# Kernel tuning notes

Measured on AMD Instinct MI355X. Metric: run time of the kernel, lower is better.

## Reference

```python
import jax, jax.numpy as jnp
import numpy as np

V, E, DZ, C = 32000, 8, 30, 10
CH = (4, 8, 8)
K = (3, 3, 3)
S = (2, 2, 1)
B, L = 512, 4096


def setup_inputs() -> dict:
    key = jax.random.key(0)
    ks = jax.random.split(key, 12)
    inp = {
        "input_ids": jax.random.randint(ks[0], (B, L), 0, V),
        "attention_mask": jnp.ones((B, L), dtype=jnp.float32),
        "z": jax.random.normal(ks[1], (DZ,), dtype=jnp.float32),
        "embed_table": jax.random.normal(ks[2], (V, E), dtype=jnp.float32),
        # ensemble-stacked frozen conv weights, torch Conv1d layout [O, I, K]
        "W1": jax.random.normal(ks[3], (DZ, CH[0], E, K[0]), dtype=jnp.float32) * 0.2,
        "b1": jax.random.normal(ks[4], (DZ, CH[0]), dtype=jnp.float32) * 0.1,
        "W2": jax.random.normal(ks[5], (DZ, CH[1], CH[0], K[1]), dtype=jnp.float32) * 0.2,
        "b2": jax.random.normal(ks[6], (DZ, CH[1]), dtype=jnp.float32) * 0.1,
        "W3": jax.random.normal(ks[7], (DZ, CH[2], CH[1], K[2]), dtype=jnp.float32) * 0.2,
        "b3": jax.random.normal(ks[8], (DZ, CH[2]), dtype=jnp.float32) * 0.1,
        "Wh": jax.random.normal(ks[9], (DZ, C, CH[2]), dtype=jnp.float32) * 0.2,
        "bh": jax.random.normal(ks[10], (DZ, C), dtype=jnp.float32) * 0.1,
    }
    return inp


def _conv1d(x, w, stride):
    # x: [B, Cin, L], w: [Cout, Cin, K]
    return jax.lax.conv_general_dilated(
        x, w, window_strides=(stride,), padding="VALID",
        dimension_numbers=("NCH", "OIH", "NCH"))


def _forward(input_ids, attention_mask, z, embed_table,
             W1, b1, W2, b2, W3, b3, Wh, bh):
    x = embed_table[input_ids]                      # [B, L, E]
    x = x * attention_mask[..., None]
    x = jnp.transpose(x, (0, 2, 1))                 # [B, E, L]

    def one_net(w1, c1, w2, c2, w3, c3, wh, ch):
        h = jax.nn.relu(_conv1d(x, w1, S[0]) + c1[None, :, None])
        h = jax.nn.relu(_conv1d(h, w2, S[1]) + c2[None, :, None])
        h = jax.nn.relu(_conv1d(h, w3, S[2]) + c3[None, :, None])
        pooled = h.mean(axis=-1)                    # [B, ch3]
        return pooled @ wh.T + ch                   # [B, C]

    pis = jax.vmap(one_net)(W1, b1, W2, b2, W3, b3, Wh, bh)  # [Dz, B, C]
    return jnp.einsum("dbc,d->bc", pis, z)          # [B, C]


def reference(input_ids, attention_mask, z, embed_table,
              W1, b1, W2, b2, W3, b3, Wh, bh):
    return _forward(input_ids, attention_mask, z, embed_table,
                    W1, b1, W2, b2, W3, b3, Wh, bh)
```

## Files before the change

### kernel.cpp

```cpp
#include <hip/hip_runtime.h>
#include <stdint.h>


typedef _Float16 f16;
typedef f16 f16x2 __attribute__((ext_vector_type(2)));
typedef f16 f16x4 __attribute__((ext_vector_type(4)));
typedef f16 f16x8 __attribute__((ext_vector_type(8)));
typedef float f32x4 __attribute__((ext_vector_type(4)));

__global__ __launch_bounds__(256) void prep_kernel(
    const int* __restrict__ ids, const float* __restrict__ mask,
    const float* __restrict__ tbl,
    const float* __restrict__ W1, const float* __restrict__ W2,
    const float* __restrict__ W3,
    f16* __restrict__ x, f16* __restrict__ a1q,
    f16* __restrict__ a2, f16* __restrict__ a3) {
  const int blk = blockIdx.x;
  if (blk < 4096) {
    const int b  = blk >> 3;
    const int l0 = ((blk & 7) * 256 + threadIdx.x) * 2;
    const int2   iv = *(const int2*)(ids + (size_t)b * 4096 + l0);
    const float2 mv = *(const float2*)(mask + (size_t)b * 4096 + l0);
    const float4* t4 = (const float4*)tbl;
    const float4 a0 = t4[(size_t)iv.x * 2], A1 = t4[(size_t)iv.x * 2 + 1];
    const float4 c0 = t4[(size_t)iv.y * 2], C1 = t4[(size_t)iv.y * 2 + 1];
    const float r0[8] = {a0.x, a0.y, a0.z, a0.w, A1.x, A1.y, A1.z, A1.w};
    const float r1[8] = {c0.x, c0.y, c0.z, c0.w, C1.x, C1.y, C1.z, C1.w};
    f16* xb = x + (size_t)b * 8 * 4096 + l0;
    #pragma unroll
    for (int e = 0; e < 8; ++e) {
      f16x2 p; p.x = (f16)(r0[e] * mv.x); p.y = (f16)(r1[e] * mv.y);
      *(f16x2*)(xb + e * 4096) = p;
    }
  } else {
    const int i = (blk - 4096) * 256 + threadIdx.x;
    if (i < 512) {
      const int g = i >> 6, l = i & 63;
      const int kg = l >> 4, col = l & 15;
      const int d = 4 * g + (col >> 2);
      f16x8 v;
      #pragma unroll
      for (int j = 0; j < 8; ++j) {
        const int e = 2 * kg + (j >> 2), tap = j & 3;
        float val = 0.0f;
        if (tap < 3 && d < 30)
          val = W1[d * 96 + (col & 3) * 24 + e * 3 + tap];
        v[j] = (f16)val;
      }
      *(f16x8*)(a1q + ((size_t)g * 64 + l) * 8) = v;
    } else if (i < 2432) {
      const int idx = i - 512, d = idx >> 6, lane = idx & 63;
      const int quad = lane >> 4, m = lane & 15;
      f16x8 v;
      #pragma unroll
      for (int j = 0; j < 8; ++j) {
        float val = 0.0f;
        if (m < 8)  { if (j < 3)           val = W2[d * 96 + m * 12 + quad * 3 + j]; }
        else        { if (j >= 2 && j < 5) val = W2[d * 96 + (m - 8) * 12 + quad * 3 + (j - 2)]; }
        v[j] = (f16)val;
      }
      *(f16x8*)(a2 + ((size_t)d * 64 + lane) * 8) = v;
    } else if (i < 4352) {
      const int idx = i - 2432, d = idx >> 6, lane = idx & 63;
      const int quad = lane >> 4, m = lane & 15;
      f16x8 v;
      #pragma unroll
      for (int j = 0; j < 8; ++j) {
        const int c2 = quad * 2 + (j >> 2), t = j & 3;
        float val = 0.0f;
        if (m < 8)  { if (t < 3)  val = W3[d * 192 + m * 24 + c2 * 3 + t]; }
        else        { if (t >= 1) val = W3[d * 192 + (m - 8) * 24 + c2 * 3 + (t - 1)]; }
        v[j] = (f16)val;
      }
      *(f16x8*)(a3 + ((size_t)d * 64 + lane) * 8) = v;
    }
  }
}

__global__ __launch_bounds__(1024, 8) void ensemble_f16_kernel(
    const f16* __restrict__ x,
    const f16* __restrict__ a1q,
    const f16* __restrict__ a2,
    const f16* __restrict__ a3,
    const float* __restrict__ z,
    const float* __restrict__ b1, const float* __restrict__ b2,
    const float* __restrict__ b3,
    const float* __restrict__ Wh, const float* __restrict__ bh,
    float* __restrict__ part)
{
  const int tid = threadIdx.x;
  const int swz = ((blockIdx.x & 7) * 512) + (blockIdx.x >> 3);
  const int b   = swz >> 3;
  const int G   = swz & 7;
  const int d_base = 4 * G;

  __shared__ __align__(16) f16 smemh[32768];
  float* red = (float*)smemh;

  const int w = tid >> 6, lane = tid & 63, quad = lane >> 4, n = lane & 15;
  const int gg = w >> 2, wv = w & 3;
  const int d  = d_base + gg;
  const int dc = d < 30 ? d : 29;

  {
    const f16x8 bw1 = *(const f16x8*)(a1q + ((size_t)G * 64 + lane) * 8);
    const int dn  = d_base + (n >> 2);
    const int dnc = dn < 30 ? dn : 29;
    const float bias = b1[dnc * 4 + (n & 3)];
    const f32x4 c1i = {bias, bias, bias, bias};
    const char* xc = (const char*)x + (size_t)b * 65536 + quad * 16384 + 4 * n;
    f16x4* h1c = (f16x4*)smemh + (n >> 2) * 2048 + (n & 3) * 512;
    const int rot1 = 5 * (n & 3);
    #pragma unroll
    for (int i = 0; i < 8; ++i) {
      const int t = w + 16 * i;
      const uint32_t o = 64u * (uint32_t)t;
      union { f16x8 v; uint32_t dw[4]; } u;
      u.dw[0] = *(const uint32_t*)(xc + o);
      u.dw[1] = *(const uint32_t*)(xc + o + 4);
      u.dw[2] = *(const uint32_t*)(xc + o + 8192);
      u.dw[3] = *(const uint32_t*)(xc + o + 8192 + 4);
      const f32x4 D = __builtin_amdgcn_mfma_f32_16x16x32_f16(u.v, bw1, c1i, 0, 0, 0);
      f16x4 p;
      p.x = (f16)fmaxf(D[0], 0.0f); p.y = (f16)fmaxf(D[1], 0.0f);
      p.z = (f16)fmaxf(D[2], 0.0f); p.w = (f16)fmaxf(D[3], 0.0f);
      const int slot = (4 * t + quad + rot1) & 511;
      h1c[slot] = p;
    }
  }
  __syncthreads();

  f32x4 Ci[8];
  {
    const f16x8 af2 = *(const f16x8*)(a2 + ((size_t)dc * 64 + lane) * 8);
    const f32x4 cinit2 = *(const f32x4*)(b2 + dc * 8 + (quad & 1) * 4);
    const f16x4* h1r = (const f16x4*)smemh + gg * 2048 + quad * 512;
    const int rot2 = 5 * quad;
    #pragma unroll
    for (int i = 0; i < 8; ++i) {
      const int t = wv + 4 * i;
      const int base = 16 * t + n;
      const f16x4 lo = h1r[(base + rot2) & 511];
      const f16x4 hi = h1r[(base + 1 + rot2) & 511];
      const f16x8 bv = __builtin_shufflevector(lo, hi, 0, 1, 2, 3, 4, 5, 6, 7);
      Ci[i] = __builtin_amdgcn_mfma_f32_16x16x32_f16(af2, bv, cinit2, 0, 0, 0);
    }
  }
  __syncthreads();

  {
    f16* h2b = smemh + gg * 8192;
    const int shift = quad >> 1;
    const int c2b   = (quad & 1) * 4;
    #pragma unroll
    for (int i = 0; i < 8; ++i) {
      const int t  = wv + 4 * i;
      const int dw = 16 * t + n;
      #pragma unroll
      for (int r = 0; r < 4; ++r) {
        const int row  = c2b + r;
        const int slot = (dw + 5 * row) & 511;
        h2b[row * 1024 + slot * 2 + shift] = (f16)fmaxf(Ci[i][r], 0.0f);
      }
    }
  }
  __syncthreads();

  float pool4[4] = {0.0f, 0.0f, 0.0f, 0.0f};
  {
    const f16x8 af3 = *(const f16x8*)(a3 + ((size_t)dc * 64 + lane) * 8);
    const f32x4 cinit3 = *(const f32x4*)(b3 + dc * 8 + (quad & 1) * 4);
    const f16* h2r = smemh + gg * 8192;
    const int c2a = quad * 2;
    const int rotA = 5 * c2a, rotB = 5 * (c2a + 1);
    #pragma unroll
    for (int i = 0; i < 8; ++i) {
      const int t  = wv + 4 * i;
      const int dw = 16 * t + n;
      union { f16x8 v; f16x2 q[4]; } u;
      u.q[0] = *(const f16x2*)(h2r + c2a * 1024       + 2 * ((dw     + rotA) & 511));
      u.q[1] = *(const f16x2*)(h2r + c2a * 1024       + 2 * ((dw + 1 + rotA) & 511));
      u.q[2] = *(const f16x2*)(h2r + (c2a + 1) * 1024 + 2 * ((dw     + rotB) & 511));
      u.q[3] = *(const f16x2*)(h2r + (c2a + 1) * 1024 + 2 * ((dw + 1 + rotB) & 511));
      const f32x4 C = __builtin_amdgcn_mfma_f32_16x16x32_f16(af3, u.v, cinit3, 0, 0, 0);
      const int pl = 32 * t + 2 * n + (quad >> 1);
      if (pl < 1021) {
        #pragma unroll
        for (int r = 0; r < 4; ++r) pool4[r] += fmaxf(C[r], 0.0f);
      }
    }
  }
  __syncthreads();

  {
    #pragma unroll
    for (int r = 0; r < 4; ++r) pool4[r] += __shfl_xor(pool4[r], 1, 64);
    #pragma unroll
    for (int r = 0; r < 4; ++r) pool4[r] += __shfl_xor(pool4[r], 2, 64);
    #pragma unroll
    for (int r = 0; r < 4; ++r) pool4[r] += __shfl_xor(pool4[r], 4, 64);
    #pragma unroll
    for (int r = 0; r < 4; ++r) pool4[r] += __shfl_xor(pool4[r], 8, 64);
    #pragma unroll
    for (int r = 0; r < 4; ++r) pool4[r] += __shfl_xor(pool4[r], 32, 64);
    if ((lane & 47) == 0) {
      const int cg = (lane >> 4) & 1;
      #pragma unroll
      for (int r = 0; r < 4; ++r)
        red[gg * 32 + wv * 8 + cg * 4 + r] = pool4[r];
    }
  }
  __syncthreads();

  if ((w & 3) == 0 && lane < 10 && d < 30) {
    float acc = bh[d * 10 + lane];
    #pragma unroll
    for (int c3 = 0; c3 < 8; ++c3) {
      const float pooled = red[gg * 32 + c3]      + red[gg * 32 + 8 + c3]
                         + red[gg * 32 + 16 + c3] + red[gg * 32 + 24 + c3];
      acc = fmaf(pooled * (1.0f / 1021.0f), Wh[d * 80 + lane * 8 + c3], acc);
    }
    part[((size_t)d * 512 + b) * 10 + lane] = z[d] * acc;
  }
}

__global__ __launch_bounds__(256) void reduce30_kernel(
    const float* __restrict__ part,
    float* __restrict__ out)
{
  const int i = blockIdx.x * 256 + threadIdx.x;
  float s = 0.0f;
  #pragma unroll
  for (int dd = 0; dd < 30; ++dd) s += part[dd * 5120 + i];
  out[i] = s;
}

__global__ __launch_bounds__(256, 6) void ensemble_kernel(
    const int* __restrict__ ids, const float* __restrict__ mask,
    const float* __restrict__ z, const float* __restrict__ tbl,
    const float* __restrict__ W1, const float* __restrict__ b1,
    const float* __restrict__ W2, const float* __restrict__ b2,
    const float* __restrict__ W3, const float* __restrict__ b3,
    const float* __restrict__ Wh, const float* __restrict__ bh,
    float* __restrict__ part)
{
  const int tid  = threadIdx.x;
  const int half = blockIdx.x & 1;
  const int bd   = blockIdx.x >> 1;
  const int b    = bd & 511;
  const int d    = bd >> 9;

  __shared__ float smem[4128];
  __shared__ float red[32];
  __shared__ float pooled[8];

  const int l_lo = half ? 1024 : 0;
  const int l_hi = half ? 2047 : 1029;
  const int j_lo = half ? 512  : 0;
  const int j_hi = half ? 1023 : 514;
  const int o_lo = half ? 512  : 0;
  const int o_hi = half ? 1021 : 512;

  const int*    idrow = ids  + (size_t)b * 4096;
  const float*  mrow  = mask + (size_t)b * 4096;
  const float4* tbl4  = (const float4*)tbl;
  const float*  w1p = W1 + d * 96;
  const float*  w2p = W2 + d * 96;
  const float*  w3p = W3 + d * 192;

  {
    float bia[4];
    #pragma unroll
    for (int c = 0; c < 4; ++c) bia[c] = b1[d * 4 + c];

    #pragma unroll 1
    for (int pass = 0; pass < 2; ++pass) {
      const int l0 = l_lo + 2 * tid + 512 * pass;
      const int p0 = 2 * l0;
      const int4   iv = *(const int4*)(idrow + p0);
      const float4 mv = *(const float4*)(mrow + p0);
      int i4; float m4;
      if (p0 + 4 < 4096) { i4 = idrow[p0 + 4]; m4 = mrow[p0 + 4]; }
      else               { i4 = 0;              m4 = 0.0f; }

      const int   pid[5] = {iv.x, iv.y, iv.z, iv.w, i4};
      const float pm[5]  = {mv.x, mv.y, mv.z, mv.w, m4};

      float a0[4], a1v[4];
      #pragma unroll
      for (int c = 0; c < 4; ++c) { a0[c] = bia[c]; a1v[c] = bia[c]; }

      #pragma unroll
      for (int q = 0; q < 5; ++q) {
        const float4 va = tbl4[(size_t)pid[q] * 2];
        const float4 vb = tbl4[(size_t)pid[q] * 2 + 1];
        const float xe[8] = {va.x * pm[q], va.y * pm[q], va.z * pm[q], va.w * pm[q],
                             vb.x * pm[q], vb.y * pm[q], vb.z * pm[q], vb.w * pm[q]};
        if (q <= 2) {
          #pragma unroll
          for (int c = 0; c < 4; ++c)
            #pragma unroll
            for (int e = 0; e < 8; ++e)
              a0[c] = fmaf(xe[e], w1p[c * 24 + e * 3 + q], a0[c]);
        }
        if (q >= 2) {
          #pragma unroll
          for (int c = 0; c < 4; ++c)
            #pragma unroll
            for (int e = 0; e < 8; ++e)
              a1v[c] = fmaf(xe[e], w1p[c * 24 + e * 3 + (q - 2)], a1v[c]);
        }
      }
      const int rel = l0 - l_lo;
      if (l0 + 1 < l_hi) {
        #pragma unroll
        for (int c = 0; c < 4; ++c)
          *(float2*)(smem + c * 1032 + rel) =
              make_float2(fmaxf(a0[c], 0.0f), fmaxf(a1v[c], 0.0f));
      } else if (l0 < l_hi) {
        #pragma unroll
        for (int c = 0; c < 4; ++c)
          smem[c * 1032 + rel] = fmaxf(a0[c], 0.0f);
      }
    }
    const int lt = l_lo + 1024 + tid;
    if (lt < l_hi) {
      float a0[4];
      #pragma unroll
      for (int c = 0; c < 4; ++c) a0[c] = bia[c];
      #pragma unroll
      for (int k = 0; k < 3; ++k) {
        const int p = 2 * lt + k;
        const int id = idrow[p];
        const float m = mrow[p];
        const float4 va = tbl4[(size_t)id * 2];
        const float4 vb = tbl4[(size_t)id * 2 + 1];
        const float xe[8] = {va.x*m, va.y*m, va.z*m, va.w*m,
                             vb.x*m, vb.y*m, vb.z*m, vb.w*m};
        #pragma unroll
        for (int cc = 0; cc < 4; ++cc)
          #pragma unroll
          for (int e = 0; e < 8; ++e)
            a0[cc] = fmaf(xe[e], w1p[cc * 24 + e * 3 + k], a0[cc]);
      }
      #pragma unroll
      for (int c = 0; c < 4; ++c)
        smem[c * 1032 + 1024 + tid] = fmaxf(a0[c], 0.0f);
    }
  }
  __syncthreads();

  float acc2[8][2], acc2t[8];
  {
    #pragma unroll
    for (int c2 = 0; c2 < 8; ++c2) {
      const float bb = b2[d * 8 + c2];
      acc2[c2][0] = bb; acc2[c2][1] = bb; acc2t[c2] = bb;
    }
    const int rel2  = 4 * tid;
    const bool tail2 = tid < (j_hi - j_lo - 512);
    #pragma unroll 1
    for (int c1 = 0; c1 < 4; ++c1) {
      float sw[8][3];
      #pragma unroll
      for (int c2 = 0; c2 < 8; ++c2)
        #pragma unroll
        for (int kk = 0; kk < 3; ++kk)
          sw[c2][kk] = w2p[c2 * 12 + c1 * 3 + kk];
      const float* hp = smem + c1 * 1032;
      const float4 h01 = *(const float4*)(hp + rel2);
      const float  h4v = hp[rel2 + 4];
      #pragma unroll
      for (int c2 = 0; c2 < 8; ++c2) {
        acc2[c2][0] = fmaf(h01.x, sw[c2][0], fmaf(h01.y, sw[c2][1],
                      fmaf(h01.z, sw[c2][2], acc2[c2][0])));
        acc2[c2][1] = fmaf(h01.z, sw[c2][0], fmaf(h01.w, sw[c2][1],
                      fmaf(h4v,   sw[c2][2], acc2[c2][1])));
      }
      if (tail2) {
        const float t0 = hp[1024 + 2 * tid], t1 = hp[1025 + 2 * tid],
                    t2 = hp[1026 + 2 * tid];
        #pragma unroll
        for (int c2 = 0; c2 < 8; ++c2)
          acc2t[c2] = fmaf(t0, sw[c2][0], fmaf(t1, sw[c2][1],
                      fmaf(t2, sw[c2][2], acc2t[c2])));
      }
    }
    #pragma unroll
    for (int c2 = 0; c2 < 8; ++c2) {
      acc2[c2][0] = fmaxf(acc2[c2][0], 0.0f);
      acc2[c2][1] = fmaxf(acc2[c2][1], 0.0f);
      acc2t[c2]   = fmaxf(acc2t[c2],   0.0f);
    }
    __syncthreads();
    const int j0 = j_lo + 2 * tid;
    const int jr = 2 * tid;
    if (j0 + 1 < j_hi) {
      #pragma unroll
      for (int c2 = 0; c2 < 8; ++c2)
        *(float2*)(smem + c2 * 516 + jr) = make_float2(acc2[c2][0], acc2[c2][1]);
    } else if (j0 < j_hi) {
      #pragma unroll
      for (int c2 = 0; c2 < 8; ++c2)
        smem[c2 * 516 + jr] = acc2[c2][0];
    }
    if (tid < (j_hi - j_lo - 512)) {
      #pragma unroll
      for (int c2 = 0; c2 < 8; ++c2)
        smem[c2 * 516 + 512 + tid] = acc2t[c2];
    }
  }
  __syncthreads();

  float acc3[8][2];
  #pragma unroll
  for (int cc = 0; cc < 8; ++cc) {
    const float bb = b3[d * 8 + cc];
    acc3[cc][0] = bb; acc3[cc][1] = bb;
  }
  {
    const int rel3 = 2 * tid;
    #pragma unroll 1
    for (int c2 = 0; c2 < 8; ++c2) {
      float sw[8][3];
      #pragma unroll
      for (int cc = 0; cc < 8; ++cc)
        #pragma unroll
        for (int kk = 0; kk < 3; ++kk)
          sw[cc][kk] = w3p[cc * 24 + c2 * 3 + kk];
      const float* hp = smem + c2 * 516;
      const float2 ha = *(const float2*)(hp + rel3);
      const float2 hb = *(const float2*)(hp + rel3 + 2);
      #pragma unroll
      for (int cc = 0; cc < 8; ++cc) {
        acc3[cc][0] = fmaf(ha.x, sw[cc][0], fmaf(ha.y, sw[cc][1],
                      fmaf(hb.x, sw[cc][2], acc3[cc][0])));
        acc3[cc][1] = fmaf(ha.y, sw[cc][0], fmaf(hb.x, sw[cc][1],
                      fmaf(hb.y, sw[cc][2], acc3[cc][1])));
      }
    }
  }
  const int i0 = o_lo + 2 * tid;
  float psum[8];
  #pragma unroll
  for (int cc = 0; cc < 8; ++cc) {
    float s = 0.0f;
    if (i0 < o_hi)     s += fmaxf(acc3[cc][0], 0.0f);
    if (i0 + 1 < o_hi) s += fmaxf(acc3[cc][1], 0.0f);
    psum[cc] = s;
  }

  const int lane = tid & 63;
  const int wid  = tid >> 6;
  #pragma unroll
  for (int c = 0; c < 8; ++c) {
    float v = psum[c];
    #pragma unroll
    for (int off = 32; off > 0; off >>= 1) v += __shfl_down(v, off, 64);
    if (lane == 0) red[wid * 8 + c] = v;
  }
  __syncthreads();
  if (tid < 8)
    pooled[tid] = red[tid] + red[8 + tid] + red[16 + tid] + red[24 + tid];
  __syncthreads();

  if (tid < 10) {
    float acc = (half == 0) ? bh[d * 10 + tid] : 0.0f;
    #pragma unroll
    for (int c3 = 0; c3 < 8; ++c3)
      acc = fmaf(pooled[c3] * (1.0f / 1021.0f), Wh[d * 80 + tid * 8 + c3], acc);
    part[(((size_t)d * 2 + half) * 512 + b) * 10 + tid] = z[d] * acc;
  }
}

__global__ __launch_bounds__(256) void reduce60_kernel(
    const float* __restrict__ part,
    float* __restrict__ out)
{
  const int i = blockIdx.x * 256 + threadIdx.x;
  float s = 0.0f;
  #pragma unroll
  for (int dd = 0; dd < 60; ++dd) s += part[dd * 5120 + i];
  out[i] = s;
}

extern "C" void kernel_launch(void* const* d_in, const int* in_sizes, int n_in,
                              void* d_out, int out_size, void* d_ws, size_t ws_size,
                              hipStream_t stream) {
  const int*   ids  = (const int*)d_in[0];
  const float* mask = (const float*)d_in[1];
  const float* z    = (const float*)d_in[2];
  const float* tbl  = (const float*)d_in[3];
  const float* W1   = (const float*)d_in[4];
  const float* b1   = (const float*)d_in[5];
  const float* W2   = (const float*)d_in[6];
  const float* b2   = (const float*)d_in[7];
  const float* W3   = (const float*)d_in[8];
  const float* b3   = (const float*)d_in[9];
  const float* Wh   = (const float*)d_in[10];
  const float* bh   = (const float*)d_in[11];
  float* out  = (float*)d_out;
  float* part = (float*)d_ws;

  const size_t part_bytes = 1228800;
  const size_t x_bytes    = (size_t)512 * 8 * 4096 * 2;
  const size_t a1_bytes   = 8192;
  const size_t a_bytes    = 30720;
  const size_t need = part_bytes + x_bytes + a1_bytes + 2 * a_bytes;

  if (ws_size >= need) {
    f16* xh  = (f16*)((char*)d_ws + part_bytes);
    f16* a1q = (f16*)((char*)d_ws + part_bytes + x_bytes);
    f16* a2  = (f16*)((char*)d_ws + part_bytes + x_bytes + a1_bytes);
    f16* a3  = (f16*)((char*)d_ws + part_bytes + x_bytes + a1_bytes + a_bytes);
    hipLaunchKernelGGL(prep_kernel, dim3(4096 + 17), dim3(256), 0, stream,
                       ids, mask, tbl, W1, W2, W3, xh, a1q, a2, a3);
    hipLaunchKernelGGL(ensemble_f16_kernel, dim3(512 * 8), dim3(1024), 0, stream,
                       xh, a1q, a2, a3, z, b1, b2, b3, Wh, bh, part);
    hipLaunchKernelGGL(reduce30_kernel, dim3(20), dim3(256), 0, stream, part, out);
  } else {
    hipLaunchKernelGGL(ensemble_kernel, dim3(512 * 30 * 2), dim3(256), 0, stream,
                       ids, mask, z, tbl, W1, b1, W2, b2, W3, b3, Wh, bh, part);
    hipLaunchKernelGGL(reduce60_kernel, dim3(20), dim3(256), 0, stream, part, out);
  }
}
```

Before: 187.2 us.

## Pre-convert embedding table to fp16 and add group term to LDS slot rotation

After: 186.3 us. No clear change (-0.5%).

```diff
diff --git a/kernel.cpp b/kernel.cpp
--- a/kernel.cpp
+++ b/kernel.cpp
@@ -8,9 +8,22 @@
 typedef f16 f16x8 __attribute__((ext_vector_type(8)));
 typedef float f32x4 __attribute__((ext_vector_type(4)));
 
+__global__ __launch_bounds__(256) void cvt_tbl_kernel(
+    const float* __restrict__ tbl, f16* __restrict__ tblh) {
+  const int i = blockIdx.x * 256 + threadIdx.x;
+  if (i < 32000) {
+    const float4* t4 = (const float4*)tbl;
+    const float4 a = t4[(size_t)i * 2], b = t4[(size_t)i * 2 + 1];
+    f16x8 v;
+    v[0] = (f16)a.x; v[1] = (f16)a.y; v[2] = (f16)a.z; v[3] = (f16)a.w;
+    v[4] = (f16)b.x; v[5] = (f16)b.y; v[6] = (f16)b.z; v[7] = (f16)b.w;
+    *(f16x8*)(tblh + (size_t)i * 8) = v;
+  }
+}
+
 __global__ __launch_bounds__(256) void prep_kernel(
     const int* __restrict__ ids, const float* __restrict__ mask,
-    const float* __restrict__ tbl,
+    const f16* __restrict__ tblh,
     const float* __restrict__ W1, const float* __restrict__ W2,
     const float* __restrict__ W3,
     f16* __restrict__ x, f16* __restrict__ a1q,
@@ -21,15 +34,13 @@
     const int l0 = ((blk & 7) * 256 + threadIdx.x) * 2;
     const int2   iv = *(const int2*)(ids + (size_t)b * 4096 + l0);
     const float2 mv = *(const float2*)(mask + (size_t)b * 4096 + l0);
-    const float4* t4 = (const float4*)tbl;
-    const float4 a0 = t4[(size_t)iv.x * 2], A1 = t4[(size_t)iv.x * 2 + 1];
-    const float4 c0 = t4[(size_t)iv.y * 2], C1 = t4[(size_t)iv.y * 2 + 1];
-    const float r0[8] = {a0.x, a0.y, a0.z, a0.w, A1.x, A1.y, A1.z, A1.w};
-    const float r1[8] = {c0.x, c0.y, c0.z, c0.w, C1.x, C1.y, C1.z, C1.w};
-    f16* xb = x + (size_t)b * 8 * 4096 + l0;
+    const f16x8 t0 = *(const f16x8*)(tblh + (size_t)iv.x * 8);
+    const f16x8 t1 = *(const f16x8*)(tblh + (size_t)iv.y * 8);
+    const f16 m0 = (f16)mv.x, m1 = (f16)mv.y;
+    f16* xb = x + (size_t)b * 32768 + l0;
     #pragma unroll
     for (int e = 0; e < 8; ++e) {
-      f16x2 p; p.x = (f16)(r0[e] * mv.x); p.y = (f16)(r1[e] * mv.y);
+      f16x2 p; p.x = t0[e] * m0; p.y = t1[e] * m1;
       *(f16x2*)(xb + e * 4096) = p;
     }
   } else {
@@ -110,7 +121,7 @@
     const f32x4 c1i = {bias, bias, bias, bias};
     const char* xc = (const char*)x + (size_t)b * 65536 + quad * 16384 + 4 * n;
     f16x4* h1c = (f16x4*)smemh + (n >> 2) * 2048 + (n & 3) * 512;
-    const int rot1 = 5 * (n & 3);
+    const int rot1 = 5 * (n & 3) + 3 * (n >> 2);
     #pragma unroll
     for (int i = 0; i < 8; ++i) {
       const int t = w + 16 * i;
@@ -135,7 +146,7 @@
     const f16x8 af2 = *(const f16x8*)(a2 + ((size_t)dc * 64 + lane) * 8);
     const f32x4 cinit2 = *(const f32x4*)(b2 + dc * 8 + (quad & 1) * 4);
     const f16x4* h1r = (const f16x4*)smemh + gg * 2048 + quad * 512;
-    const int rot2 = 5 * quad;
+    const int rot2 = 5 * quad + 3 * gg;
     #pragma unroll
     for (int i = 0; i < 8; ++i) {
       const int t = wv + 4 * i;
@@ -509,12 +520,15 @@
   const size_t need = part_bytes + x_bytes + a1_bytes + 2 * a_bytes;
 
   if (ws_size >= need) {
-    f16* xh  = (f16*)((char*)d_ws + part_bytes);
-    f16* a1q = (f16*)((char*)d_ws + part_bytes + x_bytes);
-    f16* a2  = (f16*)((char*)d_ws + part_bytes + x_bytes + a1_bytes);
-    f16* a3  = (f16*)((char*)d_ws + part_bytes + x_bytes + a1_bytes + a_bytes);
+    f16* tblh = (f16*)d_ws;
+    f16* xh   = (f16*)((char*)d_ws + part_bytes);
+    f16* a1q  = (f16*)((char*)d_ws + part_bytes + x_bytes);
+    f16* a2   = (f16*)((char*)d_ws + part_bytes + x_bytes + a1_bytes);
+    f16* a3   = (f16*)((char*)d_ws + part_bytes + x_bytes + a1_bytes + a_bytes);
+    hipLaunchKernelGGL(cvt_tbl_kernel, dim3(125), dim3(256), 0, stream,
+                       tbl, tblh);
     hipLaunchKernelGGL(prep_kernel, dim3(4096 + 17), dim3(256), 0, stream,
-                       ids, mask, tbl, W1, W2, W3, xh, a1q, a2, a3);
+                       ids, mask, tblh, W1, W2, W3, xh, a1q, a2, a3);
     hipLaunchKernelGGL(ensemble_f16_kernel, dim3(512 * 8), dim3(1024), 0, stream,
                        xh, a1q, a2, a3, z, b1, b2, b3, Wh, bh, part);
     hipLaunchKernelGGL(reduce30_kernel, dim3(20), dim3(256), 0, stream, part, out);
```
